# Optimization experiments

Hardware: AMD Instinct MI355X
Metric: run time of the kernel (lower is better)

Reference implementation:

```python
import jax, jax.numpy as jnp
import numpy as np

B, S, H = 4, 2048, 1024
NH, HD = 16, 64
LN_EPS = 1e-5


def _l2norm(x, axis=-1, eps=1e-12):
    n = jnp.sqrt(jnp.sum(x * x, axis=axis, keepdims=True))
    return x / jnp.maximum(n, eps)


def setup_inputs() -> dict:
    key = jax.random.key(0)
    ks = jax.random.split(key, 10)
    sd = 0.02
    x = jax.random.normal(ks[0], (B, S, H), jnp.float32)
    Wq = jax.random.normal(ks[1], (H, H), jnp.float32) * sd
    Wk = jax.random.normal(ks[2], (H, H), jnp.float32) * sd
    Wv = jax.random.normal(ks[3], (H, H), jnp.float32) * sd
    Wa = jax.random.normal(ks[4], (NH, H), jnp.float32) * sd
    ba = jnp.zeros((NH,), jnp.float32)
    Wb = jax.random.normal(ks[5], (NH, H), jnp.float32) * sd
    bb = jnp.zeros((NH,), jnp.float32)
    Wg = jax.random.normal(ks[6], (H, H), jnp.float32) * sd
    Wo = jax.random.normal(ks[7], (H, H), jnp.float32) * sd
    ln_g = jnp.ones((H,), jnp.float32)
    ln_b = jnp.zeros((H,), jnp.float32)
    return {"x": x, "Wq": Wq, "Wk": Wk, "Wv": Wv, "Wa": Wa, "ba": ba,
            "Wb": Wb, "bb": bb, "Wg": Wg, "Wo": Wo, "ln_g": ln_g, "ln_b": ln_b}


def _forward(x, Wq, Wk, Wv, Wa, ba, Wb, bb, Wg, Wo, ln_g, ln_b):
    q = _l2norm((x @ Wq.T).reshape(B, S, NH, HD))  # [B,S,nh,hd]
    k = _l2norm((x @ Wk.T).reshape(B, S, NH, HD))
    v = jax.nn.silu(x @ Wv.T).reshape(B, S, NH, HD)
    alpha = jax.nn.sigmoid(x @ Wa.T + ba)  # [B,S,nh]
    beta = jax.nn.sigmoid(x @ Wb.T + bb)   # [B,S,nh]

    def step(state, inp):
        a_t, b_t, k_t, v_t, q_t = inp  # a,b: [B,nh]; k,v,q: [B,nh,hd]
        a_ = a_t[:, :, None, None]
        b_ = b_t[:, :, None, None]
        kk = k_t[..., :, None] * k_t[..., None, :]  # [B,nh,hd,hd]
        state = a_ * state * (1.0 - b_ * kk) + b_ * (v_t[..., :, None] * k_t[..., None, :])
        out_t = jnp.sum(state * q_t[..., None, :], axis=-1)  # [B,nh,hd]
        return state, out_t

    # time-major xs for scan
    xs = (jnp.moveaxis(alpha, 1, 0), jnp.moveaxis(beta, 1, 0),
          jnp.moveaxis(k, 1, 0), jnp.moveaxis(v, 1, 0), jnp.moveaxis(q, 1, 0))
    state0 = jnp.zeros((B, NH, HD, HD), x.dtype)
    _, outs = jax.lax.scan(step, state0, xs)  # [S,B,nh,hd]
    out = jnp.moveaxis(outs, 0, 1).reshape(B, S, H)

    # LayerNorm over total_dim
    mu = jnp.mean(out, axis=-1, keepdims=True)
    var = jnp.var(out, axis=-1, keepdims=True)
    out = (out - mu) / jnp.sqrt(var + LN_EPS) * ln_g + ln_b

    out = out * jax.nn.silu(x @ Wg.T)
    return out @ Wo.T


def reference(x, Wq, Wk, Wv, Wa, ba, Wb, bb, Wg, Wo, ln_g, ln_b):
    return _forward(x, Wq, Wk, Wv, Wa, ba, Wb, bb, Wg, Wo, ln_g, ln_b)
```

## Files before the change

kernel.cpp:

```cpp
#include <hip/hip_runtime.h>

typedef unsigned short u16;
typedef __bf16 bf16x8 __attribute__((ext_vector_type(8)));
typedef float f32x4 __attribute__((ext_vector_type(4)));

constexpr int Bq  = 4;
constexpr int Sq  = 2048;
constexpr int Hq  = 1024;
constexpr int NHq = 16;
constexpr int HDq = 64;
constexpr int CCH = 16;
constexpr int LCH = 128;

constexpr size_t OFF_WB = 0;
constexpr size_t OFF_XB = 10485760;
constexpr size_t OFF_Q  = 27262976;
constexpr size_t OFF_K  = 60817408;
constexpr size_t OFF_V  = 94371840;
constexpr size_t OFF_G  = 127926272;
constexpr size_t OFF_AL = 161480704;
constexpr size_t OFF_BE = 162004992;
constexpr size_t OFF_P  = 162529280;
constexpr size_t OFF_O  = 179306496;

__device__ __forceinline__ u16 f2bf(float f) {
  unsigned u = __float_as_uint(f);
  u += 0x7fffu + ((u >> 16) & 1u);
  return (u16)(u >> 16);
}
__device__ __forceinline__ float sigmoidf_(float x) { return 1.f / (1.f + __expf(-x)); }

__device__ __forceinline__ void async16(const void* g, void* l) {
  __builtin_amdgcn_global_load_lds((const __attribute__((address_space(1))) void*)g,
                                   (__attribute__((address_space(3))) void*)l, 16, 0, 0);
}

__global__ __launch_bounds__(256) void cvt_x_kernel(const float* __restrict__ in, u16* __restrict__ outp) {
  const size_t i = ((size_t)blockIdx.x * 256 + threadIdx.x) * 4;
  float4 f = *(const float4*)(in + i);
  ushort4 u; u.x = f2bf(f.x); u.y = f2bf(f.y); u.z = f2bf(f.z); u.w = f2bf(f.w);
  *(ushort4*)(outp + i) = u;
}

__global__ __launch_bounds__(256) void cvt_w_kernel(const float* __restrict__ w0, const float* __restrict__ w1,
    const float* __restrict__ w2, const float* __restrict__ w3, const float* __restrict__ w4,
    u16* __restrict__ outp) {
  const int z = blockIdx.z;
  const float* src = (z == 0) ? w0 : (z == 1) ? w1 : (z == 2) ? w2 : (z == 3) ? w3 : w4;
  const size_t i = ((size_t)blockIdx.x * 256 + threadIdx.x) * 4;
  float4 f = *(const float4*)(src + i);
  ushort4 u; u.x = f2bf(f.x); u.y = f2bf(f.y); u.z = f2bf(f.z); u.w = f2bf(f.w);
  *(ushort4*)(outp + (size_t)z * (1024 * 1024) + i) = u;
}

__global__ __launch_bounds__(256) void cvt_ab_kernel(const float* __restrict__ Wa, const float* __restrict__ Wb,
    u16* __restrict__ outp) {
  const size_t i = ((size_t)blockIdx.x * 256 + threadIdx.x) * 4;
  const int row = (int)(i >> 10);
  ushort4 u;
  if (row < 32) {
    const float* src = (row < 16) ? (Wa + i) : (Wb + i - 16 * 1024);
    float4 f = *(const float4*)src;
    u.x = f2bf(f.x); u.y = f2bf(f.y); u.z = f2bf(f.z); u.w = f2bf(f.w);
  } else {
    u.x = u.y = u.z = u.w = 0;
  }
  *(ushort4*)(outp + i) = u;
}


__device__ __forceinline__ void lda4(bf16x8 af[4][2], const u16* LA, int wr, int mh, int l15, int qd, int l7) {
#pragma unroll
  for (int i = 0; i < 4; ++i)
#pragma unroll
    for (int kk = 0; kk < 2; ++kk)
      af[i][kk] = *(const bf16x8*)(LA + (wr * 128 + mh * 64 + i * 16 + l15) * 64 + (((kk * 4 + qd) ^ l7) * 8));
}
__device__ __forceinline__ void ldb2(bf16x8 bf[2][2], const u16* LB, int wc, int nh, int l15, int qd, int l7) {
#pragma unroll
  for (int j = 0; j < 2; ++j)
#pragma unroll
    for (int kk = 0; kk < 2; ++kk)
      bf[j][kk] = *(const bf16x8*)(LB + (wc * 64 + nh * 32 + j * 16 + l15) * 64 + (((kk * 4 + qd) ^ l7) * 8));
}
__device__ __forceinline__ void mm16(f32x4 acc[8][4], const bf16x8 af[4][2], const bf16x8 bf[2][2], int mh, int nh) {
#pragma unroll
  for (int i = 0; i < 4; ++i)
#pragma unroll
    for (int j = 0; j < 2; ++j) {
      f32x4 c = acc[mh * 4 + i][nh * 2 + j];
      c = __builtin_amdgcn_mfma_f32_16x16x32_bf16(af[i][0], bf[j][0], c, 0, 0, 0);
      c = __builtin_amdgcn_mfma_f32_16x16x32_bf16(af[i][1], bf[j][1], c, 0, 0, 0);
      acc[mh * 4 + i][nh * 2 + j] = c;
    }
}
__device__ __forceinline__ void stageH(u16* LD, int bufp, int mat, int h, const u16* gRow0, int kElem,
                                       int rr, int sl8, int wv) {
  const u16* s0 = gRow0 + (size_t)(h * 128 + rr) * 1024 + kElem + sl8;
  u16* d = LD + bufp * 32768 + mat * 16384 + h * 8192 + wv * 512;
  async16(s0, d);
  async16(s0 + (size_t)(64 * 1024), d + 4096);
}

template<int S1, int S2, int VM>
__device__ __forceinline__ void tile16(u16* LD, int bp, int kt,
    const u16* gA, const u16* gB, f32x4 acc[8][4], bf16x8 af[4][2], bf16x8 bf0[2][2], bf16x8 bf1[2][2],
    int wr, int wc, int l15, int qd, int l7, int rr, int sl8, int wv) {
  const u16* LA = LD + bp * 32768;
  const u16* LB = LA + 16384;
  lda4(af, LA, wr, 0, l15, qd, l7);
  ldb2(bf0, LB, wc, 0, l15, qd, l7);
  if (S1) stageH(LD, bp ^ 1, 0, 0, gA, (kt + 1) * 64, rr, sl8, wv);
  __builtin_amdgcn_s_barrier();
  asm volatile("s_waitcnt lgkmcnt(0)" ::: "memory");
  __builtin_amdgcn_sched_barrier(0);
  __builtin_amdgcn_s_setprio(1);
  mm16(acc, af, bf0, 0, 0);
  __builtin_amdgcn_s_setprio(0);
  __builtin_amdgcn_s_barrier();
  ldb2(bf1, LB, wc, 1, l15, qd, l7);
  if (S1) stageH(LD, bp ^ 1, 0, 1, gA, (kt + 1) * 64, rr, sl8, wv);
  __builtin_amdgcn_s_barrier();
  asm volatile("s_waitcnt lgkmcnt(0)" ::: "memory");
  __builtin_amdgcn_sched_barrier(0);
  __builtin_amdgcn_s_setprio(1);
  mm16(acc, af, bf1, 0, 1);
  __builtin_amdgcn_s_setprio(0);
  __builtin_amdgcn_s_barrier();
  lda4(af, LA, wr, 1, l15, qd, l7);
  if (S2) stageH(LD, bp, 1, 0, gB, (kt + 2) * 64, rr, sl8, wv);
  __builtin_amdgcn_s_barrier();
  asm volatile("s_waitcnt lgkmcnt(0)" ::: "memory");
  __builtin_amdgcn_sched_barrier(0);
  __builtin_amdgcn_s_setprio(1);
  mm16(acc, af, bf0, 1, 0);
  __builtin_amdgcn_s_setprio(0);
  __builtin_amdgcn_s_barrier();
  if (S2) stageH(LD, bp, 1, 1, gB, (kt + 2) * 64, rr, sl8, wv);
  __builtin_amdgcn_s_barrier();
  __builtin_amdgcn_sched_barrier(0);
  __builtin_amdgcn_s_setprio(1);
  mm16(acc, af, bf1, 1, 1);
  __builtin_amdgcn_s_setprio(0);
  if (VM == 4) asm volatile("s_waitcnt vmcnt(4)" ::: "memory");
  else if (VM == 0) asm volatile("s_waitcnt vmcnt(0)" ::: "memory");
  __builtin_amdgcn_s_barrier();
}

__global__ __launch_bounds__(512, 2) void gemm256(const u16* __restrict__ A, const u16* __restrict__ Wall,
    const u16* __restrict__ Wab,
    float* __restrict__ Cq, float* __restrict__ Ck, float* __restrict__ Cv, float* __restrict__ Cg,
    float* __restrict__ al, float* __restrict__ be,
    const float* __restrict__ ba, const float* __restrict__ bb, int mode) {
  __shared__ __align__(16) u16 Lds[65536];
  u16* LD = &Lds[0];
  const int tid = threadIdx.x;
  const int wv = tid >> 6, lane = tid & 63;
  const int l15 = lane & 15, qd = lane >> 4, l7 = l15 & 7;
  const int wr = wv >> 2, wc = wv & 3;
  const int rr = tid >> 3, sl8 = ((tid & 7) ^ (rr & 7)) * 8;

  int mx, ny, z;
  const u16* Wm;
  if (mode == 0) { mx = blockIdx.x & 31; ny = blockIdx.x >> 5; z = 0; Wm = Wall; }
  else if (blockIdx.x < 32) { mx = blockIdx.x; ny = 0; z = 4; Wm = Wab; }
  else {
    const int b = blockIdx.x - 32;
    mx = b & 31; ny = (b >> 5) & 3; z = b >> 7;
    Wm = Wall + (size_t)z * (1024 * 1024);
  }
  const int m0 = mx * 256, n0 = ny * 256;
  const u16* gA = A + (size_t)m0 * 1024;
  const u16* gB = Wm + (size_t)n0 * 1024;

  f32x4 acc[8][4] = {};
  bf16x8 af[4][2], bf0[2][2], bf1[2][2];

  stageH(LD, 0, 0, 0, gA, 0,  rr, sl8, wv);
  stageH(LD, 0, 0, 1, gA, 0,  rr, sl8, wv);
  stageH(LD, 0, 1, 0, gB, 0,  rr, sl8, wv);
  stageH(LD, 0, 1, 1, gB, 0,  rr, sl8, wv);
  stageH(LD, 1, 1, 0, gB, 64, rr, sl8, wv);
  stageH(LD, 1, 1, 1, gB, 64, rr, sl8, wv);
  asm volatile("s_waitcnt vmcnt(4)" ::: "memory");
  __builtin_amdgcn_s_barrier();

#pragma unroll 1
  for (int t2 = 0; t2 < 7; ++t2) {
    tile16<1, 1, 4>(LD, 0, 2 * t2,     gA, gB, acc, af, bf0, bf1, wr, wc, l15, qd, l7, rr, sl8, wv);
    tile16<1, 1, 4>(LD, 1, 2 * t2 + 1, gA, gB, acc, af, bf0, bf1, wr, wc, l15, qd, l7, rr, sl8, wv);
  }
  tile16<1, 0, 0>(LD, 0, 14, gA, gB, acc, af, bf0, bf1, wr, wc, l15, qd, l7, rr, sl8, wv);
  tile16<0, 0, -1>(LD, 1, 15, gA, gB, acc, af, bf0, bf1, wr, wc, l15, qd, l7, rr, sl8, wv);

  if (mode == 1 && z == 4) {
    if (wc == 0) {
      const float bav = ba[l15], bbv = bb[l15];
#pragma unroll
      for (int mi = 0; mi < 8; ++mi) {
        const int row = m0 + wr * 128 + mi * 16 + qd * 4;
#pragma unroll
        for (int r = 0; r < 4; ++r) {
          al[(size_t)(row + r) * 16 + l15] = sigmoidf_(acc[mi][0][r] + bav);
          be[(size_t)(row + r) * 16 + l15] = sigmoidf_(acc[mi][1][r] + bbv);
        }
      }
    }
    return;
  }
  if (mode == 1 && z <= 1) {
#pragma unroll
    for (int mi = 0; mi < 8; ++mi)
#pragma unroll
      for (int r = 0; r < 4; ++r) {
        float ss = acc[mi][0][r] * acc[mi][0][r] + acc[mi][1][r] * acc[mi][1][r]
                 + acc[mi][2][r] * acc[mi][2][r] + acc[mi][3][r] * acc[mi][3][r];
        ss += __shfl_xor(ss, 1); ss += __shfl_xor(ss, 2);
        ss += __shfl_xor(ss, 4); ss += __shfl_xor(ss, 8);
        const float rn = 1.f / fmaxf(sqrtf(ss), 1e-12f);
        acc[mi][0][r] *= rn; acc[mi][1][r] *= rn; acc[mi][2][r] *= rn; acc[mi][3][r] *= rn;
      }
  } else if (mode == 1 && z == 2) {
#pragma unroll
    for (int mi = 0; mi < 8; ++mi)
#pragma unroll
      for (int ni = 0; ni < 4; ++ni)
#pragma unroll
        for (int r = 0; r < 4; ++r)
          acc[mi][ni][r] = acc[mi][ni][r] * sigmoidf_(acc[mi][ni][r]);
  }
  float* C = (mode == 0) ? Cq : ((z == 0) ? Cq : (z == 1) ? Ck : (z == 2) ? Cv : Cg);
#pragma unroll
  for (int mi = 0; mi < 8; ++mi) {
    const int row = m0 + wr * 128 + mi * 16 + qd * 4;
#pragma unroll
    for (int ni = 0; ni < 4; ++ni) {
      const int col = n0 + wc * 64 + ni * 16 + l15;
#pragma unroll
      for (int r = 0; r < 4; ++r)
        C[(size_t)(row + r) * 1024 + col] = acc[mi][ni][r];
    }
  }
}

struct ScanLds1 { float kb[2][16 * 64]; float vb[2][16 * 64]; float ab[2][32]; };
struct ScanLds2 { float kb[2][16 * 64]; float qb[2][16 * 64]; float vb[2][16 * 64]; float ab[2][32]; };

__global__ __launch_bounds__(256, 4) void scan_p1(const float* __restrict__ k, const float* __restrict__ v,
    const float* __restrict__ al, const float* __restrict__ be,
    float* __restrict__ P, float* __restrict__ Q) {
  __shared__ ScanLds1 L;
  const int tid = threadIdx.x, wv = tid >> 6, lane = tid & 63;
  const int bh = blockIdx.x >> 4, c = blockIdx.x & 15;
  const int b = bh >> 4, h = bh & 15;
  const int rg = lane >> 3, cg = lane & 7;
  const int r0 = wv * 16 + rg * 2, c8 = cg * 8;
  const size_t base0 = ((size_t)(b * Sq + c * LCH)) * 1024 + h * 64;
  const size_t ab0   = ((size_t)(b * Sq + c * LCH)) * 16 + h;
  const int tokw = lane >> 4, seg = lane & 15;
  auto stage = [&](int tile, int bi) {
    #pragma unroll
    for (int j = 0; j < 2; ++j) {
      const int job = wv * 2 + j;
      const int arr = job >> 2, i = job & 3;
      const float* src = arr ? v : k;
      float* dst = arr ? &L.vb[bi][i * 256] : &L.kb[bi][i * 256];
      async16(src + base0 + (size_t)(tile * 16 + i * 4 + tokw) * 1024 + seg * 4, dst);
    }
    if (wv == 0 && lane < 32) {
      const int w16 = lane >> 4, tt = lane & 15;
      const float* s = w16 ? be : al;
      L.ab[bi][w16 * 16 + tt] = s[ab0 + (size_t)(tile * 16 + tt) * 16];
    }
  };
  float Pr[16], Qr[16];
  #pragma unroll
  for (int i = 0; i < 16; ++i) { Pr[i] = 1.f; Qr[i] = 0.f; }
  stage(0, 0);
  for (int tile = 0; tile < 8; ++tile) {
    __syncthreads();
    if (tile < 7) stage(tile + 1, (tile + 1) & 1);
    const int bi = tile & 1;
    const float* kbp = L.kb[bi];
    const float* vbp = L.vb[bi];
    const float* abp = L.ab[bi];
    #pragma unroll 2
    for (int tt = 0; tt < 16; ++tt) {
      const float a = abp[tt], bt = abp[16 + tt];
      float4 kcv0 = *(const float4*)(kbp + tt * 64 + c8);
      float4 kcv1 = *(const float4*)(kbp + tt * 64 + c8 + 4);
      float2 krvv = *(const float2*)(kbp + tt * 64 + r0);
      float2 vrvv = *(const float2*)(vbp + tt * 64 + r0);
      const float kcv[8] = {kcv0.x, kcv0.y, kcv0.z, kcv0.w, kcv1.x, kcv1.y, kcv1.z, kcv1.w};
      const float krv[2] = {krvv.x, krvv.y};
      const float vrv[2] = {vrvv.x, vrvv.y};
      const float abt = a * bt;
      float c1[2], c2[2];
      #pragma unroll
      for (int i = 0; i < 2; ++i) { c1[i] = abt * krv[i]; c2[i] = bt * vrv[i]; }
      #pragma unroll
      for (int i = 0; i < 2; ++i)
        #pragma unroll
        for (int j = 0; j < 8; ++j) {
          const int e = i * 8 + j;
          const float A = fmaf(-c1[i], kcv[j], a);
          Qr[e] = fmaf(A, Qr[e], c2[i] * kcv[j]);
          Pr[e] *= A;
        }
    }
  }
  const size_t pbase = ((size_t)bh * CCH + c) * 4096 + (size_t)c8;
  #pragma unroll
  for (int i = 0; i < 2; ++i) {
    const size_t pi = pbase + (size_t)(r0 + i) * 64;
    *(float4*)(P + pi)     = make_float4(Pr[i*8],   Pr[i*8+1], Pr[i*8+2], Pr[i*8+3]);
    *(float4*)(P + pi + 4) = make_float4(Pr[i*8+4], Pr[i*8+5], Pr[i*8+6], Pr[i*8+7]);
    *(float4*)(Q + pi)     = make_float4(Qr[i*8],   Qr[i*8+1], Qr[i*8+2], Qr[i*8+3]);
    *(float4*)(Q + pi + 4) = make_float4(Qr[i*8+4], Qr[i*8+5], Qr[i*8+6], Qr[i*8+7]);
  }
}

__global__ __launch_bounds__(256) void scan_comb(float* __restrict__ P, const float* __restrict__ Q) {
  const int g = blockIdx.x * 256 + threadIdx.x;
  const int elem = g & 4095;
  const int bh = g >> 12;
  float s = 0.f;
  for (int c = 0; c < CCH; ++c) {
    const size_t idx = ((size_t)bh * CCH + c) * 4096 + elem;
    const float p = P[idx], qq = Q[idx];
    P[idx] = s;
    s = fmaf(p, s, qq);
  }
}

__global__ __launch_bounds__(256, 4) void scan_p2(const float* __restrict__ q, const float* __restrict__ k,
    const float* __restrict__ v, const float* __restrict__ al, const float* __restrict__ be,
    const float* __restrict__ Pini, float* __restrict__ o) {
  __shared__ ScanLds2 L;
  const int tid = threadIdx.x, wv = tid >> 6, lane = tid & 63;
  const int bh = blockIdx.x >> 4, c = blockIdx.x & 15;
  const int b = bh >> 4, h = bh & 15;
  const int rg = lane >> 3, cg = lane & 7;
  const int r0 = wv * 16 + rg * 2, c8 = cg * 8;
  const size_t base0 = ((size_t)(b * Sq + c * LCH)) * 1024 + h * 64;
  const size_t ab0   = ((size_t)(b * Sq + c * LCH)) * 16 + h;
  const size_t pbase = ((size_t)bh * CCH + c) * 4096 + (size_t)c8;
  const int tokw = lane >> 4, seg = lane & 15;
  auto stage = [&](int tile, int bi) {
    #pragma unroll
    for (int j = 0; j < 3; ++j) {
      const int job = wv * 3 + j;
      const int arr = job >> 2, i = job & 3;
      const float* src = (arr == 0) ? k : (arr == 1) ? q : v;
      float* dst = (arr == 0) ? &L.kb[bi][i * 256] : (arr == 1) ? &L.qb[bi][i * 256]
                                                                : &L.vb[bi][i * 256];
      async16(src + base0 + (size_t)(tile * 16 + i * 4 + tokw) * 1024 + seg * 4, dst);
    }
    if (wv == 0 && lane < 32) {
      const int w16 = lane >> 4, tt = lane & 15;
      const float* s = w16 ? be : al;
      L.ab[bi][w16 * 16 + tt] = s[ab0 + (size_t)(tile * 16 + tt) * 16];
    }
  };
  float st[16];
  #pragma unroll
  for (int i = 0; i < 2; ++i) {
    float4 s0 = *(const float4*)(Pini + pbase + (size_t)(r0 + i) * 64);
    float4 s1 = *(const float4*)(Pini + pbase + (size_t)(r0 + i) * 64 + 4);
    st[i*8]   = s0.x; st[i*8+1] = s0.y; st[i*8+2] = s0.z; st[i*8+3] = s0.w;
    st[i*8+4] = s1.x; st[i*8+5] = s1.y; st[i*8+6] = s1.z; st[i*8+7] = s1.w;
  }
  stage(0, 0);
  const bool hi4 = (cg & 4);
  const int rowIdx = r0 + (cg >> 2);
  const bool doStore = ((cg & 3) == 0);
  for (int tile = 0; tile < 8; ++tile) {
    __syncthreads();
    if (tile < 7) stage(tile + 1, (tile + 1) & 1);
    const int bi = tile & 1;
    const float* kbp = L.kb[bi];
    const float* qbp = L.qb[bi];
    const float* vbp = L.vb[bi];
    const float* abp = L.ab[bi];
    #pragma unroll 2
    for (int tt = 0; tt < 16; ++tt) {
      const int t = tile * 16 + tt;
      const float a = abp[tt], bt = abp[16 + tt];
      float4 kcv0 = *(const float4*)(kbp + tt * 64 + c8);
      float4 kcv1 = *(const float4*)(kbp + tt * 64 + c8 + 4);
      float4 qcv0 = *(const float4*)(qbp + tt * 64 + c8);
      float4 qcv1 = *(const float4*)(qbp + tt * 64 + c8 + 4);
      float2 krvv = *(const float2*)(kbp + tt * 64 + r0);
      float2 vrvv = *(const float2*)(vbp + tt * 64 + r0);
      const float kcv[8] = {kcv0.x, kcv0.y, kcv0.z, kcv0.w, kcv1.x, kcv1.y, kcv1.z, kcv1.w};
      const float qcv[8] = {qcv0.x, qcv0.y, qcv0.z, qcv0.w, qcv1.x, qcv1.y, qcv1.z, qcv1.w};
      const float krv[2] = {krvv.x, krvv.y};
      const float vrv[2] = {vrvv.x, vrvv.y};
      const float abt = a * bt;
      float c1[2], c2[2];
      #pragma unroll
      for (int i = 0; i < 2; ++i) { c1[i] = abt * krv[i]; c2[i] = bt * vrv[i]; }
      float p[2];
      p[0] = 0.f; p[1] = 0.f;
      #pragma unroll
      for (int i = 0; i < 2; ++i)
        #pragma unroll
        for (int j = 0; j < 8; ++j) {
          const int e = i * 8 + j;
          const float A = fmaf(-c1[i], kcv[j], a);
          st[e] = fmaf(A, st[e], c2[i] * kcv[j]);
          p[i] = fmaf(st[e], qcv[j], p[i]);
        }
      float my    = hi4 ? p[1] : p[0];
      float other = hi4 ? p[0] : p[1];
      my += __shfl_xor(other, 4);
      my += __shfl_xor(my, 2);
      my += __shfl_xor(my, 1);
      if (doStore) o[base0 + (size_t)t * 1024 + rowIdx] = my;
    }
  }
}

__global__ __launch_bounds__(256) void ln_gate_kernel(const float* __restrict__ o, const float* __restrict__ g,
    const float* __restrict__ ln_g, const float* __restrict__ ln_b, u16* __restrict__ y) {
  const int t = blockIdx.x, tid = threadIdx.x;
  const size_t row = (size_t)t * 1024;
  float4 xv = *(const float4*)(o + row + tid * 4);
  float s  = xv.x + xv.y + xv.z + xv.w;
  float s2 = xv.x * xv.x + xv.y * xv.y + xv.z * xv.z + xv.w * xv.w;
  #pragma unroll
  for (int m = 1; m < 64; m <<= 1) { s += __shfl_xor(s, m); s2 += __shfl_xor(s2, m); }
  __shared__ float red[8];
  const int w = tid >> 6, lane = tid & 63;
  if (lane == 0) { red[w] = s; red[4 + w] = s2; }
  __syncthreads();
  s  = red[0] + red[1] + red[2] + red[3];
  s2 = red[4] + red[5] + red[6] + red[7];
  const float mu = s * (1.f / 1024.f);
  const float var = s2 * (1.f / 1024.f) - mu * mu;
  const float rstd = rsqrtf(var + 1e-5f);
  float4 gv = *(const float4*)(g + row + tid * 4);
  float4 lg = *(const float4*)(ln_g + tid * 4);
  float4 lb = *(const float4*)(ln_b + tid * 4);
  ushort4 u;
  u.x = f2bf(((xv.x - mu) * rstd * lg.x + lb.x) * (gv.x * sigmoidf_(gv.x)));
  u.y = f2bf(((xv.y - mu) * rstd * lg.y + lb.y) * (gv.y * sigmoidf_(gv.y)));
  u.z = f2bf(((xv.z - mu) * rstd * lg.z + lb.z) * (gv.z * sigmoidf_(gv.z)));
  u.w = f2bf(((xv.w - mu) * rstd * lg.w + lb.w) * (gv.w * sigmoidf_(gv.w)));
  *(ushort4*)(y + row + tid * 4) = u;
}

extern "C" void kernel_launch(void* const* d_in, const int* in_sizes, int n_in,
                              void* d_out, int out_size, void* d_ws, size_t ws_size,
                              hipStream_t stream) {
  const float* x    = (const float*)d_in[0];
  const float* Wq   = (const float*)d_in[1];
  const float* Wk   = (const float*)d_in[2];
  const float* Wv   = (const float*)d_in[3];
  const float* Wa   = (const float*)d_in[4];
  const float* ba   = (const float*)d_in[5];
  const float* Wb   = (const float*)d_in[6];
  const float* bb   = (const float*)d_in[7];
  const float* Wg   = (const float*)d_in[8];
  const float* Wo   = (const float*)d_in[9];
  const float* ln_g = (const float*)d_in[10];
  const float* ln_b = (const float*)d_in[11];
  float* out = (float*)d_out;
  char* ws = (char*)d_ws;

  u16*   wb  = (u16*)(ws + OFF_WB);
  u16*   xb  = (u16*)(ws + OFF_XB);
  float* qf  = (float*)(ws + OFF_Q);
  float* kf  = (float*)(ws + OFF_K);
  float* vf  = (float*)(ws + OFF_V);
  float* gf  = (float*)(ws + OFF_G);
  float* al  = (float*)(ws + OFF_AL);
  float* be  = (float*)(ws + OFF_BE);
  u16*   wab = (u16*)(ws + OFF_P);
  float* Pb  = (float*)(ws + OFF_P);
  float* Qc  = (float*)(ws + OFF_XB);
  float* of  = (float*)(ws + OFF_O);
  u16*   yb  = xb;

  cvt_x_kernel<<<8192, 256, 0, stream>>>(x, xb);
  cvt_w_kernel<<<dim3(1024, 1, 5), 256, 0, stream>>>(Wq, Wk, Wv, Wg, Wo, wb);
  cvt_ab_kernel<<<256, 256, 0, stream>>>(Wa, Wb, wab);
  gemm256<<<544, 512, 0, stream>>>(xb, wb, wab, qf, kf, vf, gf, al, be, ba, bb, 1);
  scan_p1<<<1024, 256, 0, stream>>>(kf, vf, al, be, Pb, Qc);
  scan_comb<<<1024, 256, 0, stream>>>(Pb, Qc);
  scan_p2<<<1024, 256, 0, stream>>>(qf, kf, vf, al, be, Pb, of);
  ln_gate_kernel<<<8192, 256, 0, stream>>>(of, gf, ln_g, ln_b, yb);
  gemm256<<<128, 512, 0, stream>>>(yb, wb + (size_t)4 * 1024 * 1024, wab,
                                   out, out, out, out, al, be, ba, bb, 0);
}
```

Before: 409.6 us.

## Split alpha/beta projection into dedicated small GEMM and prefetch scan operands

Moves the alpha/beta projection out of the big 256x256-tile GEMM, which wasted a full tile computing only 32 columns, into a small MFMA kernel. This leaves the main GEMM with exactly 512 uniform blocks. Block-to-tile mapping in both GEMM launches is permuted so concurrently running blocks group differently across the 8 index groups. The scan chunk loops are fully unrolled with software prefetch of the next step's k/q/v/alpha/beta from LDS, and the combine loop is unrolled. These changes add register pressure and an extra kernel launch.

```diff
diff --git a/kernel.cpp b/kernel.cpp
--- a/kernel.cpp
+++ b/kernel.cpp
@@ -57,15 +57,41 @@
     u16* __restrict__ outp) {
   const size_t i = ((size_t)blockIdx.x * 256 + threadIdx.x) * 4;
   const int row = (int)(i >> 10);
-  ushort4 u;
-  if (row < 32) {
-    const float* src = (row < 16) ? (Wa + i) : (Wb + i - 16 * 1024);
-    float4 f = *(const float4*)src;
-    u.x = f2bf(f.x); u.y = f2bf(f.y); u.z = f2bf(f.z); u.w = f2bf(f.w);
-  } else {
-    u.x = u.y = u.z = u.w = 0;
-  }
+  const float* src = (row < 16) ? (Wa + i) : (Wb + i - 16 * 1024);
+  float4 f = *(const float4*)src;
+  ushort4 u; u.x = f2bf(f.x); u.y = f2bf(f.y); u.z = f2bf(f.z); u.w = f2bf(f.w);
   *(ushort4*)(outp + i) = u;
+}
+
+__global__ __launch_bounds__(256) void ab_gemm(const u16* __restrict__ A, const u16* __restrict__ Wab,
+    float* __restrict__ al, float* __restrict__ be, const float* __restrict__ ba, const float* __restrict__ bb) {
+  const int tid = threadIdx.x, wv = tid >> 6, lane = tid & 63;
+  const int l15 = lane & 15, qd = lane >> 4;
+  const int m0 = blockIdx.x * 128 + wv * 32;
+  const u16* gA = A + (size_t)m0 * 1024 + qd * 8;
+  const u16* gB = Wab + (size_t)l15 * 1024 + qd * 8;
+  f32x4 acc[2][2] = {};
+#pragma unroll 4
+  for (int kt = 0; kt < 1024; kt += 32) {
+    bf16x8 a0 = *(const bf16x8*)(gA + (size_t)l15 * 1024 + kt);
+    bf16x8 a1 = *(const bf16x8*)(gA + (size_t)(16 + l15) * 1024 + kt);
+    bf16x8 b0 = *(const bf16x8*)(gB + kt);
+    bf16x8 b1 = *(const bf16x8*)(gB + 16 * 1024 + kt);
+    acc[0][0] = __builtin_amdgcn_mfma_f32_16x16x32_bf16(a0, b0, acc[0][0], 0, 0, 0);
+    acc[0][1] = __builtin_amdgcn_mfma_f32_16x16x32_bf16(a0, b1, acc[0][1], 0, 0, 0);
+    acc[1][0] = __builtin_amdgcn_mfma_f32_16x16x32_bf16(a1, b0, acc[1][0], 0, 0, 0);
+    acc[1][1] = __builtin_amdgcn_mfma_f32_16x16x32_bf16(a1, b1, acc[1][1], 0, 0, 0);
+  }
+  const float bav = ba[l15], bbv = bb[l15];
+#pragma unroll
+  for (int mi = 0; mi < 2; ++mi) {
+    const int row = m0 + mi * 16 + qd * 4;
+#pragma unroll
+    for (int r = 0; r < 4; ++r) {
+      al[(size_t)(row + r) * 16 + l15] = sigmoidf_(acc[mi][0][r] + bav);
+      be[(size_t)(row + r) * 16 + l15] = sigmoidf_(acc[mi][1][r] + bbv);
+    }
+  }
 }
 
 
@@ -148,10 +174,8 @@
 }
 
 __global__ __launch_bounds__(512, 2) void gemm256(const u16* __restrict__ A, const u16* __restrict__ Wall,
-    const u16* __restrict__ Wab,
     float* __restrict__ Cq, float* __restrict__ Ck, float* __restrict__ Cv, float* __restrict__ Cg,
-    float* __restrict__ al, float* __restrict__ be,
-    const float* __restrict__ ba, const float* __restrict__ bb, int mode) {
+    int mode) {
   __shared__ __align__(16) u16 Lds[65536];
   u16* LD = &Lds[0];
   const int tid = threadIdx.x;
@@ -162,11 +186,12 @@
 
   int mx, ny, z;
   const u16* Wm;
-  if (mode == 0) { mx = blockIdx.x & 31; ny = blockIdx.x >> 5; z = 0; Wm = Wall; }
-  else if (blockIdx.x < 32) { mx = blockIdx.x; ny = 0; z = 4; Wm = Wab; }
-  else {
-    const int b = blockIdx.x - 32;
-    mx = b & 31; ny = (b >> 5) & 3; z = b >> 7;
+  if (mode == 0) {
+    const int job = ((blockIdx.x & 7) << 4) + (blockIdx.x >> 3);
+    mx = job & 31; ny = job >> 5; z = 0; Wm = Wall;
+  } else {
+    const int job = ((blockIdx.x & 7) << 6) + (blockIdx.x >> 3);
+    mx = job & 31; ny = (job >> 5) & 3; z = job >> 7;
     Wm = Wall + (size_t)z * (1024 * 1024);
   }
   const int m0 = mx * 256, n0 = ny * 256;
@@ -193,21 +218,6 @@
   tile16<1, 0, 0>(LD, 0, 14, gA, gB, acc, af, bf0, bf1, wr, wc, l15, qd, l7, rr, sl8, wv);
   tile16<0, 0, -1>(LD, 1, 15, gA, gB, acc, af, bf0, bf1, wr, wc, l15, qd, l7, rr, sl8, wv);
 
-  if (mode == 1 && z == 4) {
-    if (wc == 0) {
-      const float bav = ba[l15], bbv = bb[l15];
-#pragma unroll
-      for (int mi = 0; mi < 8; ++mi) {
-        const int row = m0 + wr * 128 + mi * 16 + qd * 4;
-#pragma unroll
-        for (int r = 0; r < 4; ++r) {
-          al[(size_t)(row + r) * 16 + l15] = sigmoidf_(acc[mi][0][r] + bav);
-          be[(size_t)(row + r) * 16 + l15] = sigmoidf_(acc[mi][1][r] + bbv);
-        }
-      }
-    }
-    return;
-  }
   if (mode == 1 && z <= 1) {
 #pragma unroll
     for (int mi = 0; mi < 8; ++mi)
@@ -284,29 +294,36 @@
     const float* kbp = L.kb[bi];
     const float* vbp = L.vb[bi];
     const float* abp = L.ab[bi];
-    #pragma unroll 2
+    float4 kc0 = *(const float4*)(kbp + c8);
+    float4 kc1 = *(const float4*)(kbp + c8 + 4);
+    float2 krp = *(const float2*)(kbp + r0);
+    float2 vrp = *(const float2*)(vbp + r0);
+    float  ap = abp[0], btp = abp[16];
+    #pragma unroll
     for (int tt = 0; tt < 16; ++tt) {
-      const float a = abp[tt], bt = abp[16 + tt];
-      float4 kcv0 = *(const float4*)(kbp + tt * 64 + c8);
-      float4 kcv1 = *(const float4*)(kbp + tt * 64 + c8 + 4);
-      float2 krvv = *(const float2*)(kbp + tt * 64 + r0);
-      float2 vrvv = *(const float2*)(vbp + tt * 64 + r0);
-      const float kcv[8] = {kcv0.x, kcv0.y, kcv0.z, kcv0.w, kcv1.x, kcv1.y, kcv1.z, kcv1.w};
-      const float krv[2] = {krvv.x, krvv.y};
-      const float vrv[2] = {vrvv.x, vrvv.y};
-      const float abt = a * bt;
-      float c1[2], c2[2];
+      float4 nk0, nk1; float2 nkr, nvr; float na, nbt;
+      if (tt < 15) {
+        const float* kq = kbp + (tt + 1) * 64;
+        nk0 = *(const float4*)(kq + c8);
+        nk1 = *(const float4*)(kq + c8 + 4);
+        nkr = *(const float2*)(kq + r0);
+        nvr = *(const float2*)(vbp + (tt + 1) * 64 + r0);
+        na  = abp[tt + 1]; nbt = abp[16 + tt + 1];
+      }
+      const float kcv[8] = {kc0.x, kc0.y, kc0.z, kc0.w, kc1.x, kc1.y, kc1.z, kc1.w};
+      const float abt = ap * btp;
+      const float c1a = abt * krp.x, c1b = abt * krp.y;
+      const float c2a = btp * vrp.x, c2b = btp * vrp.y;
       #pragma unroll
-      for (int i = 0; i < 2; ++i) { c1[i] = abt * krv[i]; c2[i] = bt * vrv[i]; }
-      #pragma unroll
-      for (int i = 0; i < 2; ++i)
-        #pragma unroll
-        for (int j = 0; j < 8; ++j) {
-          const int e = i * 8 + j;
-          const float A = fmaf(-c1[i], kcv[j], a);
-          Qr[e] = fmaf(A, Qr[e], c2[i] * kcv[j]);
-          Pr[e] *= A;
-        }
+      for (int j = 0; j < 8; ++j) {
+        const float A0 = fmaf(-c1a, kcv[j], ap);
+        Qr[j] = fmaf(A0, Qr[j], c2a * kcv[j]);
+        Pr[j] *= A0;
+        const float A1 = fmaf(-c1b, kcv[j], ap);
+        Qr[8 + j] = fmaf(A1, Qr[8 + j], c2b * kcv[j]);
+        Pr[8 + j] *= A1;
+      }
+      if (tt < 15) { kc0 = nk0; kc1 = nk1; krp = nkr; vrp = nvr; ap = na; btp = nbt; }
     }
   }
   const size_t pbase = ((size_t)bh * CCH + c) * 4096 + (size_t)c8;
@@ -325,6 +342,7 @@
   const int elem = g & 4095;
   const int bh = g >> 12;
   float s = 0.f;
+  #pragma unroll
   for (int c = 0; c < CCH; ++c) {
     const size_t idx = ((size_t)bh * CCH + c) * 4096 + elem;
     const float p = P[idx], qq = Q[idx];
@@ -382,41 +400,50 @@
     const float* qbp = L.qb[bi];
     const float* vbp = L.vb[bi];
     const float* abp = L.ab[bi];
-    #pragma unroll 2
+    float4 kc0 = *(const float4*)(kbp + c8);
+    float4 kc1 = *(const float4*)(kbp + c8 + 4);
+    float4 qc0 = *(const float4*)(qbp + c8);
+    float4 qc1 = *(const float4*)(qbp + c8 + 4);
+    float2 krp = *(const float2*)(kbp + r0);
+    float2 vrp = *(const float2*)(vbp + r0);
+    float  ap = abp[0], btp = abp[16];
+    #pragma unroll
     for (int tt = 0; tt < 16; ++tt) {
+      float4 nk0, nk1, nq0, nq1; float2 nkr, nvr; float na, nbt;
+      if (tt < 15) {
+        const float* kq = kbp + (tt + 1) * 64;
+        const float* qq = qbp + (tt + 1) * 64;
+        nk0 = *(const float4*)(kq + c8);
+        nk1 = *(const float4*)(kq + c8 + 4);
+        nq0 = *(const float4*)(qq + c8);
+        nq1 = *(const float4*)(qq + c8 + 4);
+        nkr = *(const float2*)(kq + r0);
+        nvr = *(const float2*)(vbp + (tt + 1) * 64 + r0);
+        na  = abp[tt + 1]; nbt = abp[16 + tt + 1];
+      }
       const int t = tile * 16 + tt;
-      const float a = abp[tt], bt = abp[16 + tt];
-      float4 kcv0 = *(const float4*)(kbp + tt * 64 + c8);
-      float4 kcv1 = *(const float4*)(kbp + tt * 64 + c8 + 4);
-      float4 qcv0 = *(const float4*)(qbp + tt * 64 + c8);
-      float4 qcv1 = *(const float4*)(qbp + tt * 64 + c8 + 4);
-      float2 krvv = *(const float2*)(kbp + tt * 64 + r0);
-      float2 vrvv = *(const float2*)(vbp + tt * 64 + r0);
-      const float kcv[8] = {kcv0.x, kcv0.y, kcv0.z, kcv0.w, kcv1.x, kcv1.y, kcv1.z, kcv1.w};
-      const float qcv[8] = {qcv0.x, qcv0.y, qcv0.z, qcv0.w, qcv1.x, qcv1.y, qcv1.z, qcv1.w};
-      const float krv[2] = {krvv.x, krvv.y};
-      const float vrv[2] = {vrvv.x, vrvv.y};
-      const float abt = a * bt;
-      float c1[2], c2[2];
+      const float kcv[8] = {kc0.x, kc0.y, kc0.z, kc0.w, kc1.x, kc1.y, kc1.z, kc1.w};
+      const float qcv[8] = {qc0.x, qc0.y, qc0.z, qc0.w, qc1.x, qc1.y, qc1.z, qc1.w};
+      const float abt = ap * btp;
+      const float c1a = abt * krp.x, c1b = abt * krp.y;
+      const float c2a = btp * vrp.x, c2b = btp * vrp.y;
+      float p0 = 0.f, p1v = 0.f;
       #pragma unroll
-      for (int i = 0; i < 2; ++i) { c1[i] = abt * krv[i]; c2[i] = bt * vrv[i]; }
-      float p[2];
-      p[0] = 0.f; p[1] = 0.f;
-      #pragma unroll
-      for (int i = 0; i < 2; ++i)
-        #pragma unroll
-        for (int j = 0; j < 8; ++j) {
-          const int e = i * 8 + j;
-          const float A = fmaf(-c1[i], kcv[j], a);
-          st[e] = fmaf(A, st[e], c2[i] * kcv[j]);
-          p[i] = fmaf(st[e], qcv[j], p[i]);
-        }
-      float my    = hi4 ? p[1] : p[0];
-      float other = hi4 ? p[0] : p[1];
+      for (int j = 0; j < 8; ++j) {
+        const float A0 = fmaf(-c1a, kcv[j], ap);
+        st[j] = fmaf(A0, st[j], c2a * kcv[j]);
+        p0 = fmaf(st[j], qcv[j], p0);
+        const float A1 = fmaf(-c1b, kcv[j], ap);
+        st[8 + j] = fmaf(A1, st[8 + j], c2b * kcv[j]);
+        p1v = fmaf(st[8 + j], qcv[j], p1v);
+      }
+      float my    = hi4 ? p1v : p0;
+      float other = hi4 ? p0 : p1v;
       my += __shfl_xor(other, 4);
       my += __shfl_xor(my, 2);
       my += __shfl_xor(my, 1);
       if (doStore) o[base0 + (size_t)t * 1024 + rowIdx] = my;
+      if (tt < 15) { kc0 = nk0; kc1 = nk1; qc0 = nq0; qc1 = nq1; krp = nkr; vrp = nvr; ap = na; btp = nbt; }
     }
   }
 }
@@ -484,12 +511,12 @@
 
   cvt_x_kernel<<<8192, 256, 0, stream>>>(x, xb);
   cvt_w_kernel<<<dim3(1024, 1, 5), 256, 0, stream>>>(Wq, Wk, Wv, Wg, Wo, wb);
-  cvt_ab_kernel<<<256, 256, 0, stream>>>(Wa, Wb, wab);
-  gemm256<<<544, 512, 0, stream>>>(xb, wb, wab, qf, kf, vf, gf, al, be, ba, bb, 1);
+  cvt_ab_kernel<<<32, 256, 0, stream>>>(Wa, Wb, wab);
+  ab_gemm<<<64, 256, 0, stream>>>(xb, wab, al, be, ba, bb);
+  gemm256<<<512, 512, 0, stream>>>(xb, wb, qf, kf, vf, gf, 1);
   scan_p1<<<1024, 256, 0, stream>>>(kf, vf, al, be, Pb, Qc);
   scan_comb<<<1024, 256, 0, stream>>>(Pb, Qc);
   scan_p2<<<1024, 256, 0, stream>>>(qf, kf, vf, al, be, Pb, of);
   ln_gate_kernel<<<8192, 256, 0, stream>>>(of, gf, ln_g, ln_b, yb);
-  gemm256<<<128, 512, 0, stream>>>(yb, wb + (size_t)4 * 1024 * 1024, wab,
-                                   out, out, out, out, al, be, ba, bb, 0);
-}
+  gemm256<<<128, 512, 0, stream>>>(yb, wb + (size_t)4 * 1024 * 1024, out, out, out, out, 0);
+}
```

Result: slower. 1.504 ms (+267.2%).
